# Kernel optimization log

Hardware: AMD Instinct MI355X
Metric: run time of the kernel (lower is better)

The kernel has to match this reference:

```python
import jax, jax.numpy as jnp
import numpy as np

# NOTE: the original source omits the definitions of QSVT, quantum_lcu_block,
# QuantumSumBlock and KANLayer. We reconstruct the standard math these blocks
# implement in quantum-KAN papers/repos:
#   QSVT(x)            -> vector of Chebyshev polynomials T_1..T_D of the
#                         (squashed) input, the polynomial basis QSVT realizes.
#   quantum_lcu_block  -> linear combination of unitaries: weighted sum of the
#                         QSVT vector normalized by the LCU l1 weight norm.
#   QuantumSumBlock    -> learnable interference sum: mean_k sin(alpha_k * v).
#   KANLayer           -> Chebyshev-KAN layer: spline term (Chebyshev basis
#                         contracted with coeffs) + SiLU base branch + bias.
# Everything is fully vectorized over (B, F) instead of the original per-scalar
# Python loops.

B, F, DEG, C, KBASIS = 16384, 512, 8, 10, 8


def _cheb(x, K):
    """Chebyshev features T_1..T_K of x in (-1, 1): shape x.shape + (K,)."""
    t = jnp.arccos(jnp.clip(x, -1.0, 1.0))
    k = jnp.arange(1, K + 1, dtype=x.dtype)
    return jnp.cos(t[..., None] * k)


def setup_inputs() -> dict:
    key = jax.random.key(0)
    ks = jax.random.split(key, 6)
    return {
        "X": jax.random.normal(ks[0], (B, F), dtype=jnp.float32),
        # nn.Parameter(torch.rand(num_features, degree))
        "lcu_weights": jax.random.uniform(ks[1], (F, DEG), dtype=jnp.float32),
        # one QuantumSumBlock(degree) per feature -> (F, DEG) phases
        "sum_alpha": jax.random.normal(ks[2], (F, DEG), dtype=jnp.float32),
        # KANLayer params
        "kan_coeff": jax.random.normal(ks[3], (C, F, KBASIS), dtype=jnp.float32) * 0.1,
        "kan_base": jax.random.normal(ks[4], (C, F), dtype=jnp.float32) * 0.1,
        "kan_bias": jnp.zeros((C,), dtype=jnp.float32),
    }


def reference(X, lcu_weights, sum_alpha, kan_coeff, kan_base, kan_bias):
    # squash inputs into the open interval (-1, 1) for the Chebyshev/QSVT basis
    x = 0.99 * jnp.tanh(X)                                   # (B, F)
    # QSVT polynomial feature vector per scalar, batched: (B, F, DEG)
    qsvt = _cheb(x, lcu_weights.shape[1])
    # LCU block: weighted combination normalized by l1 norm of weights -> (B, F)
    lcu = jnp.einsum('bfd,fd->bf', qsvt, lcu_weights) / (
        jnp.sum(jnp.abs(lcu_weights), axis=-1) + 1e-8)
    # Quantum sum block: learnable sinusoidal interference sum -> (B, F)
    summed = jnp.mean(jnp.sin(lcu[..., None] * sum_alpha), axis=-1)
    # Chebyshev-KAN layer
    s = 0.99 * jnp.tanh(summed)
    phi = _cheb(s, kan_coeff.shape[2])                       # (B, F, KBASIS)
    logits = (jnp.einsum('bfk,cfk->bc', phi, kan_coeff)
              + jax.nn.silu(summed) @ kan_base.T
              + kan_bias)                                    # (B, C)
    return logits
```

## Files before the change

kernel.cpp:

```cpp
#include <hip/hip_runtime.h>
#include <hip/hip_bf16.h>

#define BATCH 16384
#define NF    512
#define DEG   8
#define NC    10
#define KB    8

#define RB     16
#define PITCH2 520
#define NT     256
#define NWAVES 4

#define CBN (NC * NF * KB)
#define BBN (NC * NF)
#define TBN (NF * DEG)

#define INV2PI 0.15915494309189535f
#define LOG2E  1.4426950408889634f

typedef __attribute__((ext_vector_type(2))) float v2f;
typedef __attribute__((ext_vector_type(8))) short bfrag;
typedef __attribute__((ext_vector_type(8))) unsigned short us8;
typedef __attribute__((ext_vector_type(4))) float f32x4;

union frag_u  { bfrag s; unsigned u[4]; };
union frag_u2 { us8 v; bfrag s; };

__device__ __forceinline__ v2f v2fma(v2f a, v2f b, v2f c) {
    return __builtin_elementwise_fma(a, b, c);
}
__device__ __forceinline__ v2f v2exp(v2f x) {
    v2f a = x * LOG2E;
    v2f r; r.x = __builtin_amdgcn_exp2f(a.x); r.y = __builtin_amdgcn_exp2f(a.y);
    return r;
}
__device__ __forceinline__ v2f v2rcp(v2f x) {
    v2f r; r.x = __builtin_amdgcn_rcpf(x.x); r.y = __builtin_amdgcn_rcpf(x.y);
    return r;
}
__device__ __forceinline__ v2f v2sin2pi(v2f x) {
    v2f r; r.x = __builtin_amdgcn_sinf(x.x); r.y = __builtin_amdgcn_sinf(x.y);
    return r;
}
__device__ __forceinline__ v2f v2tanh99(v2f x) {
    v2f e = v2exp(x + x);
    v2f r = v2rcp(e + 1.0f);
    return v2fma(r, (v2f)(-1.98f), (v2f)(0.99f));
}
__device__ __forceinline__ unsigned cvtpk2(float lo, float hi) {
    __hip_bfloat162 h = __float22bfloat162_rn(float2{lo, hi});
    unsigned u;
    __builtin_memcpy(&u, &h, sizeof(u));
    return u;
}
__device__ __forceinline__ float bf2f(unsigned short h) {
    unsigned u = ((unsigned)h) << 16;
    return __builtin_bit_cast(float, u);
}
__device__ __forceinline__ void cheb8(v2f s, v2f T[8]) {
    const v2f s2 = s + s;
    const v2f u  = v2fma(s2, s, (v2f)(-1.0f));
    const v2f u2 = u + u;
    T[0] = s;
    T[1] = u;
    T[2] = v2fma(u2, s,    -s);
    T[3] = v2fma(u2, u,    (v2f)(-1.0f));
    T[4] = v2fma(u2, T[2], -s);
    T[5] = v2fma(u2, T[3], -u);
    T[6] = v2fma(u2, T[4], -T[2]);
    T[7] = v2fma(u2, T[5], -T[3]);
}

__global__ __launch_bounds__(256) void prep_kernel(
    const float* __restrict__ coeff, const float* __restrict__ base,
    const float* __restrict__ lcu_w, const float* __restrict__ alpha,
    unsigned short* __restrict__ pk,
    float* __restrict__ wn,
    float* __restrict__ a2)
{
    const int i = blockIdx.x * 256 + threadIdx.x;
    if (i < CBN)
        pk[i] = (unsigned short)((__builtin_bit_cast(unsigned, coeff[i]) + 0x8000u) >> 16);
    else if (i < CBN + BBN)
        pk[i] = (unsigned short)((__builtin_bit_cast(unsigned, base[i - CBN]) + 0x8000u) >> 16);
    if (i < NF) {
        float w[DEG], d = 1e-8f;
#pragma unroll
        for (int k = 0; k < DEG; ++k) { w[k] = lcu_w[i * DEG + k]; d += fabsf(w[k]); }
        const float rd = 1.0f / d;
#pragma unroll
        for (int k = 0; k < DEG; ++k) {
            wn[i * DEG + k] = w[k] * rd;
            a2[i * DEG + k] = alpha[i * DEG + k] * INV2PI;
        }
    }
}

__global__ __launch_bounds__(NT, 4) void qkan_kernel(
    const float* __restrict__ X,
    const float* __restrict__ wn,
    const float* __restrict__ a2,
    const unsigned short* __restrict__ pk,
    const float* __restrict__ bias,
    float* __restrict__ out)
{
    __shared__ unsigned short s_s[RB * PITCH2];
    __shared__ unsigned short s_l[RB * PITCH2];
    __shared__ float s_red[NWAVES * RB * 16];

    const int t    = threadIdx.x;
    const int row0 = blockIdx.x * RB;

    {
        const int fA = t * 2;
        v2f W[DEG], A[DEG];
        {
            const float4 w0 = *(const float4*)(wn + fA * DEG);
            const float4 w1 = *(const float4*)(wn + fA * DEG + 4);
            const float4 w2 = *(const float4*)(wn + fA * DEG + 8);
            const float4 w3 = *(const float4*)(wn + fA * DEG + 12);
            const float4 a0 = *(const float4*)(a2 + fA * DEG);
            const float4 a1 = *(const float4*)(a2 + fA * DEG + 4);
            const float4 a3 = *(const float4*)(a2 + fA * DEG + 8);
            const float4 a4 = *(const float4*)(a2 + fA * DEG + 12);
            const float wf0[8] = {w0.x,w0.y,w0.z,w0.w,w1.x,w1.y,w1.z,w1.w};
            const float wf1[8] = {w2.x,w2.y,w2.z,w2.w,w3.x,w3.y,w3.z,w3.w};
            const float af0[8] = {a0.x,a0.y,a0.z,a0.w,a1.x,a1.y,a1.z,a1.w};
            const float af1[8] = {a3.x,a3.y,a3.z,a3.w,a4.x,a4.y,a4.z,a4.w};
#pragma unroll
            for (int d = 0; d < DEG; ++d) {
                W[d] = (v2f){wf0[d], wf1[d]};
                A[d] = (v2f){af0[d], af1[d]};
            }
        }

#pragma unroll 4
        for (int r = 0; r < RB; ++r) {
            const v2f xv = *(const v2f*)(X + (row0 + r) * NF + fA);
            const v2f x  = v2tanh99(xv);
            v2f T[8];
            cheb8(x, T);
            v2f n0 = W[0] * T[0];
            v2f n1 = W[1] * T[1];
            n0 = v2fma(W[2], T[2], n0);  n1 = v2fma(W[3], T[3], n1);
            n0 = v2fma(W[4], T[4], n0);  n1 = v2fma(W[5], T[5], n1);
            n0 = v2fma(W[6], T[6], n0);  n1 = v2fma(W[7], T[7], n1);
            const v2f lcu = n0 + n1;
            v2f sn[8];
#pragma unroll
            for (int d = 0; d < DEG; ++d)
                sn[d] = v2sin2pi(lcu * A[d]);
            const v2f ss = ((sn[0] + sn[1]) + (sn[2] + sn[3]))
                         + ((sn[4] + sn[5]) + (sn[6] + sn[7]));
            const v2f sm = ss * 0.125f;

            const v2f E  = v2exp(sm);
            const v2f s  = v2fma(v2rcp(v2fma(E, E, (v2f)(1.0f))),
                                 (v2f)(-1.98f), (v2f)(0.99f));
            const v2f si = sm * E * v2rcp(E + 1.0f);

            *(unsigned*)(&s_s[r * PITCH2 + fA]) = cvtpk2(s.x, s.y);
            *(unsigned*)(&s_l[r * PITCH2 + fA]) = cvtpk2(si.x, si.y);
        }
    }
    __syncthreads();

    const int lane = t & 63;
    const int wave = __builtin_amdgcn_readfirstlane(t >> 6);
    const int n    = lane & 15;
    const int q    = lane >> 4;
    const int ncl  = (n < NC) ? n : (NC - 1);
    const int fw   = wave * 128;

    const unsigned short* cb = pk;
    const unsigned short* bb = pk + CBN;
    const unsigned short* cbase = cb + (ncl * NF + fw) * KB;

    f32x4 acc0 = {0.f, 0.f, 0.f, 0.f};
    f32x4 acc1 = {0.f, 0.f, 0.f, 0.f};

#pragma unroll 4
    for (int kp = 0; kp < 16; ++kp) {
        const bfrag b0 = *(const bfrag*)(cbase + (kp * 8 + q) * KB);
        const bfrag b1 = *(const bfrag*)(cbase + (kp * 8 + 4 + q) * KB);

        const float sA = bf2f(s_s[n * PITCH2 + fw + kp * 8 + q]);
        const float sB = bf2f(s_s[n * PITCH2 + fw + kp * 8 + 4 + q]);
        v2f T[8];
        cheb8((v2f){sA, sB}, T);
        frag_u fa0, fa1;
#pragma unroll
        for (int i = 0; i < 4; ++i) {
            fa0.u[i] = cvtpk2(T[2 * i].x, T[2 * i + 1].x);
            fa1.u[i] = cvtpk2(T[2 * i].y, T[2 * i + 1].y);
        }
        acc0 = __builtin_amdgcn_mfma_f32_16x16x32_bf16(fa0.s, b0, acc0, 0, 0, 0);
        acc1 = __builtin_amdgcn_mfma_f32_16x16x32_bf16(fa1.s, b1, acc1, 0, 0, 0);
    }

#pragma unroll
    for (int kt2 = 0; kt2 < 4; ++kt2) {
        const bfrag b = *(const bfrag*)(bb + ncl * NF + fw + kt2 * 32 + q * 8);
        frag_u2 fa;
        fa.v = *(const us8*)(&s_l[n * PITCH2 + fw + kt2 * 32 + q * 8]);
        if (kt2 & 1)
            acc1 = __builtin_amdgcn_mfma_f32_16x16x32_bf16(fa.s, b, acc1, 0, 0, 0);
        else
            acc0 = __builtin_amdgcn_mfma_f32_16x16x32_bf16(fa.s, b, acc0, 0, 0, 0);
    }

    const f32x4 acc = acc0 + acc1;
#pragma unroll
    for (int i = 0; i < 4; ++i)
        s_red[wave * (RB * 16) + (q * 4 + i) * 16 + n] = acc[i];
    __syncthreads();

    if (t < RB * NC) {
        const int r = t / NC;
        const int c = t - r * NC;
        float v = bias[c];
#pragma unroll
        for (int w = 0; w < NWAVES; ++w)
            v += s_red[w * (RB * 16) + r * 16 + c];
        out[(row0 + r) * NC + c] = v;
    }
}

extern "C" void kernel_launch(void* const* d_in, const int* in_sizes, int n_in,
                              void* d_out, int out_size, void* d_ws, size_t ws_size,
                              hipStream_t stream) {
    const float* X      = (const float*)d_in[0];
    const float* lcu_w  = (const float*)d_in[1];
    const float* alpha  = (const float*)d_in[2];
    const float* coeff  = (const float*)d_in[3];
    const float* base   = (const float*)d_in[4];
    const float* bias   = (const float*)d_in[5];
    float* out = (float*)d_out;
    unsigned short* pk = (unsigned short*)d_ws;
    float* wn = (float*)(pk + CBN + BBN);
    float* a2 = wn + TBN;

    prep_kernel<<<(CBN + BBN + 255) / 256, 256, 0, stream>>>(
        coeff, base, lcu_w, alpha, pk, wn, a2);
    qkan_kernel<<<BATCH / RB, NT, 0, stream>>>(X, wn, a2, pk, bias, out);
}
```

Measured before the change: 100.1 us.

## Split fused kernel into elementwise pass and MFMA GEMM pass via global buffers

The single kernel that computed the elementwise QSVT/LCU/sum stage into LDS and then ran the MFMA contraction is split into two kernels. The first writes bf16 s and silu planes to global workspace, and the second reads them back for the matrix-core contraction. This removes LDS usage and the intra-block barrier so each phase can be scheduled with its own occupancy. In exchange it adds an extra launch and a write plus read of two BxF bf16 planes through global memory, and needs a larger workspace.

```diff
diff --git a/kernel.cpp b/kernel.cpp
--- a/kernel.cpp
+++ b/kernel.cpp
@@ -8,13 +8,13 @@
 #define KB    8
 
 #define RB     16
-#define PITCH2 520
 #define NT     256
 #define NWAVES 4
 
 #define CBN (NC * NF * KB)
 #define BBN (NC * NF)
 #define TBN (NF * DEG)
+#define PLANE (BATCH * NF)
 
 #define INV2PI 0.15915494309189535f
 #define LOG2E  1.4426950408889634f
@@ -97,75 +97,79 @@
     }
 }
 
-__global__ __launch_bounds__(NT, 4) void qkan_kernel(
+__global__ __launch_bounds__(NT) void ew_kernel(
     const float* __restrict__ X,
     const float* __restrict__ wn,
     const float* __restrict__ a2,
+    unsigned short* __restrict__ gs,
+    unsigned short* __restrict__ gl)
+{
+    const int t    = threadIdx.x;
+    const int row0 = blockIdx.x * RB;
+    const int fA   = t * 2;
+
+    v2f W[DEG], A[DEG];
+    {
+        const float4 w0 = *(const float4*)(wn + fA * DEG);
+        const float4 w1 = *(const float4*)(wn + fA * DEG + 4);
+        const float4 w2 = *(const float4*)(wn + fA * DEG + 8);
+        const float4 w3 = *(const float4*)(wn + fA * DEG + 12);
+        const float4 a0 = *(const float4*)(a2 + fA * DEG);
+        const float4 a1 = *(const float4*)(a2 + fA * DEG + 4);
+        const float4 a3 = *(const float4*)(a2 + fA * DEG + 8);
+        const float4 a4 = *(const float4*)(a2 + fA * DEG + 12);
+        const float wf0[8] = {w0.x,w0.y,w0.z,w0.w,w1.x,w1.y,w1.z,w1.w};
+        const float wf1[8] = {w2.x,w2.y,w2.z,w2.w,w3.x,w3.y,w3.z,w3.w};
+        const float af0[8] = {a0.x,a0.y,a0.z,a0.w,a1.x,a1.y,a1.z,a1.w};
+        const float af1[8] = {a3.x,a3.y,a3.z,a3.w,a4.x,a4.y,a4.z,a4.w};
+#pragma unroll
+        for (int d = 0; d < DEG; ++d) {
+            W[d] = (v2f){wf0[d], wf1[d]};
+            A[d] = (v2f){af0[d], af1[d]};
+        }
+    }
+
+#pragma unroll 4
+    for (int r = 0; r < RB; ++r) {
+        const v2f xv = *(const v2f*)(X + (row0 + r) * NF + fA);
+        const v2f x  = v2tanh99(xv);
+        v2f T[8];
+        cheb8(x, T);
+        v2f n0 = W[0] * T[0];
+        v2f n1 = W[1] * T[1];
+        n0 = v2fma(W[2], T[2], n0);  n1 = v2fma(W[3], T[3], n1);
+        n0 = v2fma(W[4], T[4], n0);  n1 = v2fma(W[5], T[5], n1);
+        n0 = v2fma(W[6], T[6], n0);  n1 = v2fma(W[7], T[7], n1);
+        const v2f lcu = n0 + n1;
+        v2f sn[8];
+#pragma unroll
+        for (int d = 0; d < DEG; ++d)
+            sn[d] = v2sin2pi(lcu * A[d]);
+        const v2f ss = ((sn[0] + sn[1]) + (sn[2] + sn[3]))
+                     + ((sn[4] + sn[5]) + (sn[6] + sn[7]));
+        const v2f sm = ss * 0.125f;
+
+        const v2f E  = v2exp(sm);
+        const v2f s  = v2fma(v2rcp(v2fma(E, E, (v2f)(1.0f))),
+                             (v2f)(-1.98f), (v2f)(0.99f));
+        const v2f si = sm * E * v2rcp(E + 1.0f);
+
+        *(unsigned*)(&gs[(row0 + r) * NF + fA]) = cvtpk2(s.x, s.y);
+        *(unsigned*)(&gl[(row0 + r) * NF + fA]) = cvtpk2(si.x, si.y);
+    }
+}
+
+__global__ __launch_bounds__(NT, 4) void gemm_kernel(
+    const unsigned short* __restrict__ gs,
+    const unsigned short* __restrict__ gl,
     const unsigned short* __restrict__ pk,
     const float* __restrict__ bias,
     float* __restrict__ out)
 {
-    __shared__ unsigned short s_s[RB * PITCH2];
-    __shared__ unsigned short s_l[RB * PITCH2];
     __shared__ float s_red[NWAVES * RB * 16];
 
     const int t    = threadIdx.x;
     const int row0 = blockIdx.x * RB;
-
-    {
-        const int fA = t * 2;
-        v2f W[DEG], A[DEG];
-        {
-            const float4 w0 = *(const float4*)(wn + fA * DEG);
-            const float4 w1 = *(const float4*)(wn + fA * DEG + 4);
-            const float4 w2 = *(const float4*)(wn + fA * DEG + 8);
-            const float4 w3 = *(const float4*)(wn + fA * DEG + 12);
-            const float4 a0 = *(const float4*)(a2 + fA * DEG);
-            const float4 a1 = *(const float4*)(a2 + fA * DEG + 4);
-            const float4 a3 = *(const float4*)(a2 + fA * DEG + 8);
-            const float4 a4 = *(const float4*)(a2 + fA * DEG + 12);
-            const float wf0[8] = {w0.x,w0.y,w0.z,w0.w,w1.x,w1.y,w1.z,w1.w};
-            const float wf1[8] = {w2.x,w2.y,w2.z,w2.w,w3.x,w3.y,w3.z,w3.w};
-            const float af0[8] = {a0.x,a0.y,a0.z,a0.w,a1.x,a1.y,a1.z,a1.w};
-            const float af1[8] = {a3.x,a3.y,a3.z,a3.w,a4.x,a4.y,a4.z,a4.w};
-#pragma unroll
-            for (int d = 0; d < DEG; ++d) {
-                W[d] = (v2f){wf0[d], wf1[d]};
-                A[d] = (v2f){af0[d], af1[d]};
-            }
-        }
-
-#pragma unroll 4
-        for (int r = 0; r < RB; ++r) {
-            const v2f xv = *(const v2f*)(X + (row0 + r) * NF + fA);
-            const v2f x  = v2tanh99(xv);
-            v2f T[8];
-            cheb8(x, T);
-            v2f n0 = W[0] * T[0];
-            v2f n1 = W[1] * T[1];
-            n0 = v2fma(W[2], T[2], n0);  n1 = v2fma(W[3], T[3], n1);
-            n0 = v2fma(W[4], T[4], n0);  n1 = v2fma(W[5], T[5], n1);
-            n0 = v2fma(W[6], T[6], n0);  n1 = v2fma(W[7], T[7], n1);
-            const v2f lcu = n0 + n1;
-            v2f sn[8];
-#pragma unroll
-            for (int d = 0; d < DEG; ++d)
-                sn[d] = v2sin2pi(lcu * A[d]);
-            const v2f ss = ((sn[0] + sn[1]) + (sn[2] + sn[3]))
-                         + ((sn[4] + sn[5]) + (sn[6] + sn[7]));
-            const v2f sm = ss * 0.125f;
-
-            const v2f E  = v2exp(sm);
-            const v2f s  = v2fma(v2rcp(v2fma(E, E, (v2f)(1.0f))),
-                                 (v2f)(-1.98f), (v2f)(0.99f));
-            const v2f si = sm * E * v2rcp(E + 1.0f);
-
-            *(unsigned*)(&s_s[r * PITCH2 + fA]) = cvtpk2(s.x, s.y);
-            *(unsigned*)(&s_l[r * PITCH2 + fA]) = cvtpk2(si.x, si.y);
-        }
-    }
-    __syncthreads();
-
     const int lane = t & 63;
     const int wave = __builtin_amdgcn_readfirstlane(t >> 6);
     const int n    = lane & 15;
@@ -176,6 +180,8 @@
     const unsigned short* cb = pk;
     const unsigned short* bb = pk + CBN;
     const unsigned short* cbase = cb + (ncl * NF + fw) * KB;
+    const unsigned short* srow  = gs + (row0 + n) * NF + fw;
+    const unsigned short* lrow  = gl + (row0 + n) * NF + fw;
 
     f32x4 acc0 = {0.f, 0.f, 0.f, 0.f};
     f32x4 acc1 = {0.f, 0.f, 0.f, 0.f};
@@ -185,8 +191,8 @@
         const bfrag b0 = *(const bfrag*)(cbase + (kp * 8 + q) * KB);
         const bfrag b1 = *(const bfrag*)(cbase + (kp * 8 + 4 + q) * KB);
 
-        const float sA = bf2f(s_s[n * PITCH2 + fw + kp * 8 + q]);
-        const float sB = bf2f(s_s[n * PITCH2 + fw + kp * 8 + 4 + q]);
+        const float sA = bf2f(srow[kp * 8 + q]);
+        const float sB = bf2f(srow[kp * 8 + 4 + q]);
         v2f T[8];
         cheb8((v2f){sA, sB}, T);
         frag_u fa0, fa1;
@@ -203,7 +209,7 @@
     for (int kt2 = 0; kt2 < 4; ++kt2) {
         const bfrag b = *(const bfrag*)(bb + ncl * NF + fw + kt2 * 32 + q * 8);
         frag_u2 fa;
-        fa.v = *(const us8*)(&s_l[n * PITCH2 + fw + kt2 * 32 + q * 8]);
+        fa.v = *(const us8*)(lrow + kt2 * 32 + q * 8);
         if (kt2 & 1)
             acc1 = __builtin_amdgcn_mfma_f32_16x16x32_bf16(fa.s, b, acc1, 0, 0, 0);
         else
@@ -237,11 +243,15 @@
     const float* base   = (const float*)d_in[4];
     const float* bias   = (const float*)d_in[5];
     float* out = (float*)d_out;
-    unsigned short* pk = (unsigned short*)d_ws;
+
+    unsigned short* gs = (unsigned short*)d_ws;
+    unsigned short* gl = gs + PLANE;
+    unsigned short* pk = gl + PLANE;
     float* wn = (float*)(pk + CBN + BBN);
     float* a2 = wn + TBN;
 
     prep_kernel<<<(CBN + BBN + 255) / 256, 256, 0, stream>>>(
         coeff, base, lcu_w, alpha, pk, wn, a2);
-    qkan_kernel<<<BATCH / RB, NT, 0, stream>>>(X, wn, a2, pk, bias, out);
-}
+    ew_kernel<<<BATCH / RB, NT, 0, stream>>>(X, wn, a2, gs, gl);
+    gemm_kernel<<<BATCH / RB, NT, 0, stream>>>(gs, gl, pk, bias, out);
+}
```

Result: slower. 124.7 us (+24.6%).
